# Kernel tuning notes

Measured on AMD Instinct MI355X. Metric: run time of the kernel, lower is better.

Reference implementation:

```python
import jax, jax.numpy as jnp
import numpy as np

DIM = 1024
HEADS = 16
HEAD_DIM = DIM // HEADS
HIDDEN = int(DIM * 4.0)
EPS = 1e-5


def setup_inputs() -> dict:
    key = jax.random.key(0)
    ks = jax.random.split(key, 16)
    s = 0.02
    inp = {
        'x': jax.random.normal(ks[0], (2, 2048, DIM), dtype=jnp.float32),
        'g1': jnp.ones((DIM,), jnp.float32),
        'b1': jnp.zeros((DIM,), jnp.float32),
        'Wq': jax.random.normal(ks[1], (DIM, DIM)) * s,
        'bq': jnp.zeros((DIM,), jnp.float32),
        'Wk': jax.random.normal(ks[2], (DIM, DIM)) * s,
        'bk': jnp.zeros((DIM,), jnp.float32),
        'Wv': jax.random.normal(ks[3], (DIM, DIM)) * s,
        'bv': jnp.zeros((DIM,), jnp.float32),
        'Wo': jax.random.normal(ks[4], (DIM, DIM)) * s,
        'bo': jnp.zeros((DIM,), jnp.float32),
        'g2': jnp.ones((DIM,), jnp.float32),
        'b2': jnp.zeros((DIM,), jnp.float32),
        'W1': jax.random.normal(ks[5], (DIM, HIDDEN)) * s,
        'bf1': jnp.zeros((HIDDEN,), jnp.float32),
        'W2': jax.random.normal(ks[6], (HIDDEN, DIM)) * s,
        'bf2': jnp.zeros((DIM,), jnp.float32),
    }
    return inp


def _layernorm(x, g, b):
    mu = jnp.mean(x, axis=-1, keepdims=True)
    var = jnp.mean((x - mu) ** 2, axis=-1, keepdims=True)
    return (x - mu) * jax.lax.rsqrt(var + EPS) * g + b


def _block(x, g1, b1, Wq, bq, Wk, bk, Wv, bv, Wo, bo, g2, b2, W1, bf1, W2, bf2):
    B, N, C = x.shape
    h = _layernorm(x, g1, b1)
    # project and split heads: [B, H, N, D]
    q = (h @ Wq + bq).reshape(B, N, HEADS, HEAD_DIM).transpose(0, 2, 1, 3)
    k = (h @ Wk + bk).reshape(B, N, HEADS, HEAD_DIM).transpose(0, 2, 1, 3)
    v = (h @ Wv + bv).reshape(B, N, HEADS, HEAD_DIM).transpose(0, 2, 1, 3)
    scale = HEAD_DIM ** -0.5
    attn = jnp.einsum('bhqd,bhkd->bhqk', q, k) * scale
    attn = jax.nn.softmax(attn, axis=-1)
    o = jnp.einsum('bhqk,bhkd->bhqd', attn, v)
    o = o.transpose(0, 2, 1, 3).reshape(B, N, C)
    x = x + (o @ Wo + bo)
    h = _layernorm(x, g2, b2)
    h = jax.nn.gelu(h @ W1 + bf1, approximate=False)
    x = x + (h @ W2 + bf2)
    return x


def reference(x, g1, b1, Wq, bq, Wk, bk, Wv, bv, Wo, bo, g2, b2, W1, bf1, W2, bf2):
    return _block(x, g1, b1, Wq, bq, Wk, bk, Wv, bv, Wo, bo, g2, b2, W1, bf1, W2, bf2)
```

## Files before the change

kernel.cpp:

```cpp
#include <hip/hip_runtime.h>
#include <hip/hip_bf16.h>
#include <math.h>


typedef unsigned short ushort_t;
typedef short short8 __attribute__((ext_vector_type(8)));
typedef float f32x4 __attribute__((ext_vector_type(4)));

#define TOKENS 4096
#define SEQ    2048
#define DIMC   1024
#define HID    4096

__device__ __forceinline__ float bf2f(ushort_t u) {
    union { float f; unsigned int u; } c; c.u = ((unsigned int)u) << 16; return c.f;
}
__device__ __forceinline__ ushort_t f2bf(float f) {
    union { float f; unsigned int u; } c; c.f = f;
    unsigned int u = c.u;
    unsigned int r = u + 0x7fffu + ((u >> 16) & 1u);
    return (ushort_t)(r >> 16);
}
__device__ __forceinline__ float gelu_f(float x) {
    const float y = 0.79788456080286536f * (x + 0.044715f * x * x * x);
    const float t = __expf(-2.0f * fabsf(y));
    const float th = (1.0f - t) / (1.0f + t);
    return 0.5f * x * (1.0f + copysignf(th, y));
}
__device__ __forceinline__ float load_elem(const void* p, size_t i, int isbf) {
    return isbf ? bf2f(((const ushort_t*)p)[i]) : ((const float*)p)[i];
}

__global__ __launch_bounds__(256) void detect_dtype(
    const ushort_t* __restrict__ x, int* __restrict__ flag)
{
    __shared__ int bad;
    if (threadIdx.x == 0) bad = 0;
    __syncthreads();
    for (int i = threadIdx.x; i < 4096; i += 256) {
        float v = bf2f(x[i]);
        if (!(fabsf(v) <= 1e6f)) bad = 1;
    }
    __syncthreads();
    if (threadIdx.x == 0) { flag[0] = (bad == 0) ? 1 : 0; flag[1] = 1; }
}

__global__ __launch_bounds__(256) void transpose_conv(
    const void* __restrict__ in, ushort_t* __restrict__ out, int K, int N,
    const int* __restrict__ flag)
{
    __shared__ ushort_t tile[32][33];
    const int isbf = *flag;
    const int kb = blockIdx.y * 32, nb = blockIdx.x * 32;
    const int tx = threadIdx.x & 31, ty = threadIdx.x >> 5;
    for (int i = 0; i < 4; i++) {
        int k = kb + ty + i * 8;
        tile[ty + i * 8][tx] = f2bf(load_elem(in, (size_t)k * N + nb + tx, isbf));
    }
    __syncthreads();
    for (int i = 0; i < 4; i++) {
        int n = nb + ty + i * 8;
        out[(size_t)n * K + kb + tx] = tile[tx][ty + i * 8];
    }
}

__global__ __launch_bounds__(256) void transpose_conv4(
    const void* __restrict__ w0, const void* __restrict__ w1,
    const void* __restrict__ w2, const void* __restrict__ w3,
    ushort_t* __restrict__ outbase, const int* __restrict__ flag)
{
    __shared__ ushort_t tile[32][33];
    const int isbf = *flag;
    const int z = blockIdx.z;
    const void* in = z == 0 ? w0 : (z == 1 ? w1 : (z == 2 ? w2 : w3));
    ushort_t* out = outbase + (size_t)z * DIMC * DIMC;
    const int kb = blockIdx.y * 32, nb = blockIdx.x * 32;
    const int tx = threadIdx.x & 31, ty = threadIdx.x >> 5;
    for (int i = 0; i < 4; i++) {
        int k = kb + ty + i * 8;
        tile[ty + i * 8][tx] = f2bf(load_elem(in, (size_t)k * DIMC + nb + tx, isbf));
    }
    __syncthreads();
    for (int i = 0; i < 4; i++) {
        int n = nb + ty + i * 8;
        out[(size_t)n * DIMC + kb + tx] = tile[tx][ty + i * 8];
    }
}

__global__ __launch_bounds__(256) void transpose_v(
    const ushort_t* __restrict__ in, ushort_t* __restrict__ out)
{
    __shared__ ushort_t tile[32][33];
    const int z = blockIdx.z;
    const ushort_t* src = in  + (size_t)z * SEQ * DIMC;
    ushort_t*       dst = out + (size_t)z * DIMC * SEQ;
    const int kb = blockIdx.y * 32, nb = blockIdx.x * 32;
    const int tx = threadIdx.x & 31, ty = threadIdx.x >> 5;
    for (int i = 0; i < 4; i++) {
        int k = kb + ty + i * 8;
        tile[ty + i * 8][tx] = src[(size_t)k * DIMC + nb + tx];
    }
    __syncthreads();
    for (int i = 0; i < 4; i++) {
        int n = nb + ty + i * 8;
        dst[(size_t)n * SEQ + kb + tx] = tile[tx][ty + i * 8];
    }
}

template<int INMODE>
__global__ __launch_bounds__(256) void ln_kernel(
    const void* __restrict__ in, const void* __restrict__ g,
    const void* __restrict__ b, const int* __restrict__ flag,
    ushort_t* __restrict__ out)
{
    const int isbf = *flag;
    const int t = blockIdx.x;
    const int tid = threadIdx.x;
    const size_t base = (size_t)t * DIMC;
    float v[4];
    for (int i = 0; i < 4; i++) {
        int idx = tid + i * 256;
        v[i] = (INMODE == 1) ? ((const float*)in)[base + idx]
                             : load_elem(in, base + idx, isbf);
    }
    float s  = v[0] + v[1] + v[2] + v[3];
    float s2 = v[0]*v[0] + v[1]*v[1] + v[2]*v[2] + v[3]*v[3];
    for (int off = 1; off < 64; off <<= 1) {
        s  += __shfl_xor(s,  off);
        s2 += __shfl_xor(s2, off);
    }
    __shared__ float red[8];
    const int wave = tid >> 6, lane = tid & 63;
    if (lane == 0) { red[wave] = s; red[wave + 4] = s2; }
    __syncthreads();
    s  = red[0] + red[1] + red[2] + red[3];
    s2 = red[4] + red[5] + red[6] + red[7];
    const float mu  = s * (1.0f / DIMC);
    const float var = s2 * (1.0f / DIMC) - mu * mu;
    const float inv = rsqrtf(fmaxf(var, 0.f) + 1e-5f);
    for (int i = 0; i < 4; i++) {
        int idx = tid + i * 256;
        float o = (v[i] - mu) * inv * load_elem(g, idx, isbf) + load_elem(b, idx, isbf);
        out[base + idx] = f2bf(o);
    }
}

template<int BN, int RES, int ACT, int OUTF>
__global__ __launch_bounds__(256) void gemm_bt(
    const ushort_t* __restrict__ A, const ushort_t* __restrict__ BT,
    const void* __restrict__ bias0, const void* __restrict__ bias1,
    const void* __restrict__ bias2, const void* __restrict__ resid,
    void* __restrict__ out0, void* __restrict__ out1, void* __restrict__ out2,
    int M, int N, int K, int Ksub, const int* __restrict__ flag)
{
    constexpr int BM   = 128;
    constexpr int JF   = BN / 32;
    constexpr int ASEG = BM / 16;
    constexpr int SPW  = (BM + BN) / 64;
    __shared__ __align__(16) ushort_t As[BM][32];
    __shared__ __align__(16) ushort_t Bs[BN][32];
    const int isbf = *flag;
    const int tid = threadIdx.x, lane = tid & 63, wave = tid >> 6;
    const int m0 = blockIdx.y * BM, n0 = blockIdx.x * BN;
    const int wm = (wave & 1) * 64;
    const int wn = (wave >> 1) * (BN / 2);
    const int lm = lane & 15, quad = lane >> 4;

    const void* biasp = bias0;
    void* outp = out0;
    int nout = N;
    int colmask = 0x7fffffff;
    if (OUTF == 3) {
        const int sel = n0 >> 10;
        biasp = sel == 0 ? bias0 : (sel == 1 ? bias1 : bias2);
        outp  = sel == 0 ? out0  : (sel == 1 ? out1  : out2);
        nout = 1024; colmask = 1023;
    }
    int kbeg = 0;
    if (OUTF == 4) {
        kbeg = blockIdx.z * Ksub;
        outp = blockIdx.z ? out1 : out0;
    }

    f32x4 acc[4][JF];
    for (int i = 0; i < 4; i++)
        for (int j = 0; j < JF; j++)
            acc[i][j] = (f32x4){0.f, 0.f, 0.f, 0.f};

    const int lrow = lane >> 2;
    const int lcol = (lane & 3) * 8;

    for (int k0 = kbeg; k0 < kbeg + Ksub; k0 += 32) {
#pragma unroll
        for (int s = 0; s < SPW; s++) {
            const int seg = wave * SPW + s;
            const ushort_t* gp;
            ushort_t* lp;
            if (seg < ASEG) {
                gp = &A[(size_t)(m0 + seg * 16 + lrow) * K + k0 + lcol];
                lp = &As[seg * 16][0];
            } else {
                gp = &BT[(size_t)(n0 + (seg - ASEG) * 16 + lrow) * K + k0 + lcol];
                lp = &Bs[(seg - ASEG) * 16][0];
            }
            __builtin_amdgcn_global_load_lds(
                (const __attribute__((address_space(1))) unsigned int*)gp,
                (__attribute__((address_space(3))) unsigned int*)lp, 16, 0, 0);
        }
        __syncthreads();
        short8 af[4], bfr[JF];
#pragma unroll
        for (int i = 0; i < 4; i++) af[i] = *(const short8*)&As[wm + i * 16 + lm][quad * 8];
#pragma unroll
        for (int j = 0; j < JF; j++) bfr[j] = *(const short8*)&Bs[wn + j * 16 + lm][quad * 8];
#pragma unroll
        for (int i = 0; i < 4; i++)
#pragma unroll
            for (int j = 0; j < JF; j++)
                acc[i][j] = __builtin_amdgcn_mfma_f32_16x16x32_bf16(af[i], bfr[j], acc[i][j], 0, 0, 0);
        __syncthreads();
    }

    for (int j = 0; j < JF; j++) {
        const int col  = n0 + wn + j * 16 + lm;
        const int colo = col & colmask;
        const float bv = (OUTF == 4) ? 0.f : load_elem(biasp, colo, isbf);
        for (int i = 0; i < 4; i++) {
            const int rbase = m0 + wm + i * 16 + quad * 4;
            for (int r = 0; r < 4; r++) {
                const size_t oi = (size_t)(rbase + r) * nout + colo;
                float v2 = acc[i][j][r] + bv;
                if (ACT == 1) v2 = gelu_f(v2);
                if (RES == 1) v2 += load_elem(resid, oi, isbf);
                if (RES == 2) v2 += ((const float*)resid)[oi];
                if (OUTF == 1 || OUTF == 4) { ((float*)outp)[oi] = v2; }
                else if (OUTF == 2) {
                    if (isbf) ((ushort_t*)outp)[oi] = f2bf(v2);
                    else      ((float*)outp)[oi] = v2;
                }
                else                { ((ushort_t*)outp)[oi] = f2bf(v2); }
            }
        }
    }
}

__global__ __launch_bounds__(256) void splitk_reduce(
    const float* __restrict__ p0, const float* __restrict__ p1,
    const void* __restrict__ bias, const float* __restrict__ resid,
    void* __restrict__ out, const int* __restrict__ flag)
{
    const int isbf = *flag;
    const size_t i = ((size_t)blockIdx.x * 256 + threadIdx.x) * 4;
    const float4 a = *(const float4*)&p0[i];
    const float4 b = *(const float4*)&p1[i];
    const float4 r = *(const float4*)&resid[i];
    const int col = (int)(i & 1023);
    float v[4];
    v[0] = a.x + b.x + r.x + load_elem(bias, col + 0, isbf);
    v[1] = a.y + b.y + r.y + load_elem(bias, col + 1, isbf);
    v[2] = a.z + b.z + r.z + load_elem(bias, col + 2, isbf);
    v[3] = a.w + b.w + r.w + load_elem(bias, col + 3, isbf);
    if (isbf) {
        unsigned int lo = (unsigned int)f2bf(v[0]) | ((unsigned int)f2bf(v[1]) << 16);
        unsigned int hi = (unsigned int)f2bf(v[2]) | ((unsigned int)f2bf(v[3]) << 16);
        *(uint2*)&((ushort_t*)out)[i] = make_uint2(lo, hi);
    } else {
        *(float4*)&((float*)out)[i] = make_float4(v[0], v[1], v[2], v[3]);
    }
}

__global__ __launch_bounds__(256) void attn_kernel(
    const ushort_t* __restrict__ q, const ushort_t* __restrict__ k,
    const ushort_t* __restrict__ vt, ushort_t* __restrict__ o)
{
    const int bh = blockIdx.x;
    const int b  = bh >> 4, h = bh & 15;
    const int q0 = blockIdx.y * 64;
    const int tid = threadIdx.x, lane = tid & 63, wave = tid >> 6;
    const int lm = lane & 15, quad = lane >> 4;

    __shared__ ushort_t Qs[64][72];
    __shared__ ushort_t Ks[64][72];
    __shared__ ushort_t Vt[64][72];
    __shared__ ushort_t Ps[4][16][72];

    const size_t base  = ((size_t)b * SEQ) * DIMC + h * 64;
    const size_t vbase = ((size_t)b * DIMC + h * 64) * SEQ;

    {
        const int er0 = (tid * 8) >> 6;
        const int ec0 = (tid * 8) & 63;
        for (int half = 0; half < 2; half++) {
            const int r = er0 + half * 32;
            short8 qq = *(const short8*)&q[base + (size_t)(q0 + r) * DIMC + ec0];
            short8 qs;
            for (int i = 0; i < 8; i++)
                qs[i] = (short)f2bf(bf2f((ushort_t)qq[i]) * 0.18033688011112042f);
            *(short8*)&Qs[r][ec0] = qs;
        }
    }
    __syncthreads();

    short8 qf[2];
    qf[0] = *(const short8*)&Qs[wave * 16 + lm][quad * 8];
    qf[1] = *(const short8*)&Qs[wave * 16 + lm][quad * 8 + 32];

    short8 onef;
    for (int i = 0; i < 8; i++) onef[i] = (short)0x3F80;

    f32x4 oacc[4], lacc;
    for (int j = 0; j < 4; j++) oacc[j] = (f32x4){0.f, 0.f, 0.f, 0.f};
    lacc = (f32x4){0.f, 0.f, 0.f, 0.f};

    const int er = (tid * 8) >> 6;
    const int ec = (tid * 8) & 63;
    const int dd = tid >> 2;
    const int kg = tid & 3;

    for (int kt = 0; kt < SEQ / 64; kt++) {
        __syncthreads();
        for (int half = 0; half < 2; half++) {
            const int r = er + half * 32;
            *(short8*)&Ks[r][ec] =
                *(const short8*)&k[base + (size_t)(kt * 64 + r) * DIMC + ec];
        }
        {
            const size_t vsrc = vbase + (size_t)dd * SEQ + kt * 64 + kg * 16;
            *(short8*)&Vt[dd][kg * 16]     = *(const short8*)&vt[vsrc];
            *(short8*)&Vt[dd][kg * 16 + 8] = *(const short8*)&vt[vsrc + 8];
        }
        __syncthreads();

        f32x4 st[4];
        for (int j = 0; j < 4; j++) st[j] = (f32x4){0.f, 0.f, 0.f, 0.f};
        for (int ks = 0; ks < 2; ks++) {
            for (int j = 0; j < 4; j++) {
                short8 kf = *(const short8*)&Ks[j * 16 + lm][quad * 8 + ks * 32];
                st[j] = __builtin_amdgcn_mfma_f32_16x16x32_bf16(kf, qf[ks], st[j], 0, 0, 0);
            }
        }

        for (int j = 0; j < 4; j++) {
            unsigned int u0 = __float_as_uint(exp2f(st[j][0]));
            unsigned int u1 = __float_as_uint(exp2f(st[j][1]));
            unsigned int u2 = __float_as_uint(exp2f(st[j][2]));
            unsigned int u3 = __float_as_uint(exp2f(st[j][3]));
            unsigned int lo = (u1 & 0xffff0000u) | (u0 >> 16);
            unsigned int hi = (u3 & 0xffff0000u) | (u2 >> 16);
            *(uint2*)&Ps[wave][lm][j * 16 + quad * 4] = make_uint2(lo, hi);
        }

        for (int ks = 0; ks < 2; ks++) {
            short8 pf = *(const short8*)&Ps[wave][lm][quad * 8 + ks * 32];
            lacc = __builtin_amdgcn_mfma_f32_16x16x32_bf16(pf, onef, lacc, 0, 0, 0);
            for (int j = 0; j < 4; j++) {
                short8 vf = *(const short8*)&Vt[j * 16 + lm][quad * 8 + ks * 32];
                oacc[j] = __builtin_amdgcn_mfma_f32_16x16x32_bf16(pf, vf, oacc[j], 0, 0, 0);
            }
        }
    }

    float rinv[4];
    for (int r = 0; r < 4; r++) rinv[r] = 1.0f / fmaxf(lacc[r], 1e-30f);

    for (int j = 0; j < 4; j++)
        for (int r = 0; r < 4; r++) {
            const int row = q0 + wave * 16 + quad * 4 + r;
            o[base + (size_t)row * DIMC + j * 16 + lm] = f2bf(oacc[j][r] * rinv[r]);
        }
}

extern "C" void kernel_launch(void* const* d_in, const int* in_sizes, int n_in,
                              void* d_out, int out_size, void* d_ws, size_t ws_size,
                              hipStream_t stream)
{
    const void* x   = d_in[0];
    const void* g1  = d_in[1];
    const void* b1  = d_in[2];
    const void* Wq  = d_in[3];
    const void* bq  = d_in[4];
    const void* Wk  = d_in[5];
    const void* bk  = d_in[6];
    const void* Wv  = d_in[7];
    const void* bv  = d_in[8];
    const void* Wo  = d_in[9];
    const void* bo  = d_in[10];
    const void* g2  = d_in[11];
    const void* b2  = d_in[12];
    const void* W1  = d_in[13];
    const void* bf1 = d_in[14];
    const void* W2  = d_in[15];
    const void* bf2 = d_in[16];

    const size_t SZ_TOKD_BF = (size_t)TOKENS * DIMC * 2;
    const size_t SZ_TOKD_F  = (size_t)TOKENS * DIMC * 4;
    const size_t SZ_W_SQ    = (size_t)DIMC * DIMC * 2;
    const size_t SZ_W_FF    = (size_t)DIMC * HID * 2;
    const size_t SZ_FF1     = (size_t)TOKENS * HID * 2;

    char* ws = (char*)d_ws;
    size_t off = 0;
    int*      flag = (int*)(ws + off);       off += 256;
    ushort_t* h    = (ushort_t*)(ws + off);  off += SZ_TOKD_BF;
    ushort_t* qb   = (ushort_t*)(ws + off);  off += SZ_TOKD_BF;
    ushort_t* kb_  = (ushort_t*)(ws + off);  off += SZ_TOKD_BF;
    ushort_t* vb   = (ushort_t*)(ws + off);  off += SZ_TOKD_BF;
    ushort_t* vtg  = (ushort_t*)(ws + off);  off += SZ_TOKD_BF;
    float*    x1f  = (float*)qb;
    ushort_t* ao   = vb;
    float*    p0   = (float*)vb;
    ushort_t* wqt  = (ushort_t*)(ws + off);  off += SZ_W_SQ;
    ushort_t* wkt  = (ushort_t*)(ws + off);  off += SZ_W_SQ;
    ushort_t* wvt  = (ushort_t*)(ws + off);  off += SZ_W_SQ;
    ushort_t* wot  = (ushort_t*)(ws + off);  off += SZ_W_SQ;
    ushort_t* w1t  = (ushort_t*)(ws + off);  off += SZ_W_FF;
    ushort_t* w2t  = (ushort_t*)(ws + off);  off += SZ_W_FF;
    ushort_t* ff1  = (ushort_t*)(ws + off);  off += SZ_FF1;
    float*    p1   = (float*)(ws + off);     off += SZ_TOKD_F;
    if (ws_size < off) return;

    (void)wkt; (void)wvt;

    detect_dtype<<<1, 256, 0, stream>>>((const ushort_t*)x, flag);

    transpose_conv4<<<dim3(32, 32, 4), 256, 0, stream>>>(Wq, Wk, Wv, Wo, wqt, flag);
    transpose_conv<<<dim3(128, 32), 256, 0, stream>>>(W1, w1t, DIMC, HID, flag);
    transpose_conv<<<dim3(32, 128), 256, 0, stream>>>(W2, w2t, HID, DIMC, flag);

    ln_kernel<0><<<TOKENS, 256, 0, stream>>>(x, g1, b1, flag, h);

    gemm_bt<128, 0, 0, 3><<<dim3(24, 32), 256, 0, stream>>>(
        h, wqt, bq, bk, bv, nullptr, qb, kb_, vb, TOKENS, 3072, DIMC, DIMC, flag);

    transpose_v<<<dim3(32, 64, 2), 256, 0, stream>>>(vb, vtg);

    attn_kernel<<<dim3(32, 32), 256, 0, stream>>>(qb, kb_, vtg, ao);

    gemm_bt<64, 1, 0, 1><<<dim3(16, 32), 256, 0, stream>>>(
        ao, wot, bo, nullptr, nullptr, x, x1f, nullptr, nullptr, TOKENS, DIMC, DIMC, DIMC, flag);

    ln_kernel<1><<<TOKENS, 256, 0, stream>>>(x1f, g2, b2, flag, h);

    gemm_bt<128, 0, 1, 0><<<dim3(32, 32), 256, 0, stream>>>(
        h, w1t, bf1, nullptr, nullptr, nullptr, ff1, nullptr, nullptr, TOKENS, HID, DIMC, DIMC, flag);

    gemm_bt<64, 0, 0, 4><<<dim3(16, 32, 2), 256, 0, stream>>>(
        ff1, w2t, nullptr, nullptr, nullptr, nullptr, p0, p1, nullptr,
        TOKENS, DIMC, HID, HID / 2, flag);

    splitk_reduce<<<TOKENS * DIMC / 1024, 256, 0, stream>>>(p0, p1, bf2, x1f, d_out, flag);
}
```

Measured before the change: 448.8 us.

## Fuse V transpose into QKV GEMM epilogue, enlarge attention tile, prefetch K/V

The QKV GEMM epilogue now writes V directly in transposed [B, C, S] layout, which removes the separate transpose_v kernel and its extra pass over memory. The attention kernel processes 128 queries per block (32 per wave), so each K/V tile loaded into LDS is reused across twice as many queries. It also prefetches the next K/V tile into registers while computing on the current one, and uses the hardware exp2 intrinsic. The two FFN weight transposes are merged into a single launch. Together these raise register pressure and halve the attention grid, which can lower occupancy.

```diff
diff --git a/kernel.cpp b/kernel.cpp
--- a/kernel.cpp
+++ b/kernel.cpp
@@ -43,25 +43,6 @@
     }
     __syncthreads();
     if (threadIdx.x == 0) { flag[0] = (bad == 0) ? 1 : 0; flag[1] = 1; }
-}
-
-__global__ __launch_bounds__(256) void transpose_conv(
-    const void* __restrict__ in, ushort_t* __restrict__ out, int K, int N,
-    const int* __restrict__ flag)
-{
-    __shared__ ushort_t tile[32][33];
-    const int isbf = *flag;
-    const int kb = blockIdx.y * 32, nb = blockIdx.x * 32;
-    const int tx = threadIdx.x & 31, ty = threadIdx.x >> 5;
-    for (int i = 0; i < 4; i++) {
-        int k = kb + ty + i * 8;
-        tile[ty + i * 8][tx] = f2bf(load_elem(in, (size_t)k * N + nb + tx, isbf));
-    }
-    __syncthreads();
-    for (int i = 0; i < 4; i++) {
-        int n = nb + ty + i * 8;
-        out[(size_t)n * K + kb + tx] = tile[tx][ty + i * 8];
-    }
 }
 
 __global__ __launch_bounds__(256) void transpose_conv4(
@@ -87,23 +68,30 @@
     }
 }
 
-__global__ __launch_bounds__(256) void transpose_v(
-    const ushort_t* __restrict__ in, ushort_t* __restrict__ out)
+__global__ __launch_bounds__(256) void transpose_ff(
+    const void* __restrict__ W1, const void* __restrict__ W2,
+    ushort_t* __restrict__ w1t, ushort_t* __restrict__ w2t,
+    const int* __restrict__ flag)
 {
     __shared__ ushort_t tile[32][33];
+    const int isbf = *flag;
     const int z = blockIdx.z;
-    const ushort_t* src = in  + (size_t)z * SEQ * DIMC;
-    ushort_t*       dst = out + (size_t)z * DIMC * SEQ;
-    const int kb = blockIdx.y * 32, nb = blockIdx.x * 32;
+    const void* in = z ? W2 : W1;
+    ushort_t* out = z ? w2t : w1t;
+    const int K = z ? HID : DIMC;
+    const int N = z ? DIMC : HID;
+    const int bx = z ? blockIdx.y : blockIdx.x;
+    const int by = z ? blockIdx.x : blockIdx.y;
+    const int kb = by * 32, nb = bx * 32;
     const int tx = threadIdx.x & 31, ty = threadIdx.x >> 5;
     for (int i = 0; i < 4; i++) {
         int k = kb + ty + i * 8;
-        tile[ty + i * 8][tx] = src[(size_t)k * DIMC + nb + tx];
+        tile[ty + i * 8][tx] = f2bf(load_elem(in, (size_t)k * N + nb + tx, isbf));
     }
     __syncthreads();
     for (int i = 0; i < 4; i++) {
         int n = nb + ty + i * 8;
-        dst[(size_t)n * SEQ + kb + tx] = tile[tx][ty + i * 8];
+        out[(size_t)n * K + kb + tx] = tile[tx][ty + i * 8];
     }
 }
 
@@ -170,8 +158,9 @@
     void* outp = out0;
     int nout = N;
     int colmask = 0x7fffffff;
+    int sel = 0;
     if (OUTF == 3) {
-        const int sel = n0 >> 10;
+        sel = n0 >> 10;
         biasp = sel == 0 ? bias0 : (sel == 1 ? bias1 : bias2);
         outp  = sel == 0 ? out0  : (sel == 1 ? out1  : out2);
         nout = 1024; colmask = 1023;
@@ -219,6 +208,24 @@
             for (int j = 0; j < JF; j++)
                 acc[i][j] = __builtin_amdgcn_mfma_f32_16x16x32_bf16(af[i], bfr[j], acc[i][j], 0, 0, 0);
         __syncthreads();
+    }
+
+    if (OUTF == 3 && sel == 2) {
+        for (int j = 0; j < JF; j++) {
+            const int colo = (n0 + wn + j * 16 + lm) & 1023;
+            const float bv = load_elem(biasp, colo, isbf);
+            for (int i = 0; i < 4; i++) {
+                const int token = m0 + wm + i * 16 + quad * 4;
+                const int bb = token >> 11, ss = token & 2047;
+                unsigned int lo = (unsigned int)f2bf(acc[i][j][0] + bv)
+                                | ((unsigned int)f2bf(acc[i][j][1] + bv) << 16);
+                unsigned int hi = (unsigned int)f2bf(acc[i][j][2] + bv)
+                                | ((unsigned int)f2bf(acc[i][j][3] + bv) << 16);
+                *(uint2*)&((ushort_t*)outp)[(size_t)((bb << 10) + colo) * SEQ + ss] =
+                    make_uint2(lo, hi);
+            }
+        }
+        return;
     }
 
     for (int j = 0; j < JF; j++) {
@@ -275,14 +282,14 @@
 {
     const int bh = blockIdx.x;
     const int b  = bh >> 4, h = bh & 15;
-    const int q0 = blockIdx.y * 64;
+    const int q0 = blockIdx.y * 128;
     const int tid = threadIdx.x, lane = tid & 63, wave = tid >> 6;
     const int lm = lane & 15, quad = lane >> 4;
 
-    __shared__ ushort_t Qs[64][72];
+    __shared__ ushort_t Qs[128][72];
     __shared__ ushort_t Ks[64][72];
     __shared__ ushort_t Vt[64][72];
-    __shared__ ushort_t Ps[4][16][72];
+    __shared__ ushort_t Ps[4][32][72];
 
     const size_t base  = ((size_t)b * SEQ) * DIMC + h * 64;
     const size_t vbase = ((size_t)b * DIMC + h * 64) * SEQ;
@@ -290,7 +297,7 @@
     {
         const int er0 = (tid * 8) >> 6;
         const int ec0 = (tid * 8) & 63;
-        for (int half = 0; half < 2; half++) {
+        for (int half = 0; half < 4; half++) {
             const int r = er0 + half * 32;
             short8 qq = *(const short8*)&q[base + (size_t)(q0 + r) * DIMC + ec0];
             short8 qs;
@@ -301,73 +308,94 @@
     }
     __syncthreads();
 
-    short8 qf[2];
-    qf[0] = *(const short8*)&Qs[wave * 16 + lm][quad * 8];
-    qf[1] = *(const short8*)&Qs[wave * 16 + lm][quad * 8 + 32];
+    short8 qf[2][2];
+    for (int qh = 0; qh < 2; qh++)
+        for (int ks = 0; ks < 2; ks++)
+            qf[qh][ks] = *(const short8*)&Qs[wave * 32 + qh * 16 + lm][quad * 8 + ks * 32];
 
     short8 onef;
     for (int i = 0; i < 8; i++) onef[i] = (short)0x3F80;
 
-    f32x4 oacc[4], lacc;
-    for (int j = 0; j < 4; j++) oacc[j] = (f32x4){0.f, 0.f, 0.f, 0.f};
-    lacc = (f32x4){0.f, 0.f, 0.f, 0.f};
+    f32x4 oacc[4][2], lacc[2];
+    for (int j = 0; j < 4; j++)
+        for (int qh = 0; qh < 2; qh++) oacc[j][qh] = (f32x4){0.f, 0.f, 0.f, 0.f};
+    lacc[0] = (f32x4){0.f, 0.f, 0.f, 0.f};
+    lacc[1] = (f32x4){0.f, 0.f, 0.f, 0.f};
 
     const int er = (tid * 8) >> 6;
     const int ec = (tid * 8) & 63;
     const int dd = tid >> 2;
     const int kg = tid & 3;
 
+    short8 kreg0, kreg1, vreg0, vreg1;
+    {
+        kreg0 = *(const short8*)&k[base + (size_t)(er) * DIMC + ec];
+        kreg1 = *(const short8*)&k[base + (size_t)(er + 32) * DIMC + ec];
+        const size_t vsrc = vbase + (size_t)dd * SEQ + kg * 16;
+        vreg0 = *(const short8*)&vt[vsrc];
+        vreg1 = *(const short8*)&vt[vsrc + 8];
+    }
+
     for (int kt = 0; kt < SEQ / 64; kt++) {
         __syncthreads();
-        for (int half = 0; half < 2; half++) {
-            const int r = er + half * 32;
-            *(short8*)&Ks[r][ec] =
-                *(const short8*)&k[base + (size_t)(kt * 64 + r) * DIMC + ec];
-        }
-        {
-            const size_t vsrc = vbase + (size_t)dd * SEQ + kt * 64 + kg * 16;
-            *(short8*)&Vt[dd][kg * 16]     = *(const short8*)&vt[vsrc];
-            *(short8*)&Vt[dd][kg * 16 + 8] = *(const short8*)&vt[vsrc + 8];
-        }
+        *(short8*)&Ks[er][ec]          = kreg0;
+        *(short8*)&Ks[er + 32][ec]     = kreg1;
+        *(short8*)&Vt[dd][kg * 16]     = vreg0;
+        *(short8*)&Vt[dd][kg * 16 + 8] = vreg1;
         __syncthreads();
-
-        f32x4 st[4];
-        for (int j = 0; j < 4; j++) st[j] = (f32x4){0.f, 0.f, 0.f, 0.f};
+        if (kt + 1 < SEQ / 64) {
+            const int kn = (kt + 1) * 64;
+            kreg0 = *(const short8*)&k[base + (size_t)(kn + er) * DIMC + ec];
+            kreg1 = *(const short8*)&k[base + (size_t)(kn + er + 32) * DIMC + ec];
+            const size_t vsrc = vbase + (size_t)dd * SEQ + kn + kg * 16;
+            vreg0 = *(const short8*)&vt[vsrc];
+            vreg1 = *(const short8*)&vt[vsrc + 8];
+        }
+
+        f32x4 st[4][2];
+        for (int j = 0; j < 4; j++)
+            for (int qh = 0; qh < 2; qh++) st[j][qh] = (f32x4){0.f, 0.f, 0.f, 0.f};
         for (int ks = 0; ks < 2; ks++) {
             for (int j = 0; j < 4; j++) {
                 short8 kf = *(const short8*)&Ks[j * 16 + lm][quad * 8 + ks * 32];
-                st[j] = __builtin_amdgcn_mfma_f32_16x16x32_bf16(kf, qf[ks], st[j], 0, 0, 0);
-            }
-        }
-
-        for (int j = 0; j < 4; j++) {
-            unsigned int u0 = __float_as_uint(exp2f(st[j][0]));
-            unsigned int u1 = __float_as_uint(exp2f(st[j][1]));
-            unsigned int u2 = __float_as_uint(exp2f(st[j][2]));
-            unsigned int u3 = __float_as_uint(exp2f(st[j][3]));
-            unsigned int lo = (u1 & 0xffff0000u) | (u0 >> 16);
-            unsigned int hi = (u3 & 0xffff0000u) | (u2 >> 16);
-            *(uint2*)&Ps[wave][lm][j * 16 + quad * 4] = make_uint2(lo, hi);
-        }
+                for (int qh = 0; qh < 2; qh++)
+                    st[j][qh] = __builtin_amdgcn_mfma_f32_16x16x32_bf16(kf, qf[qh][ks], st[j][qh], 0, 0, 0);
+            }
+        }
+
+        for (int j = 0; j < 4; j++)
+            for (int qh = 0; qh < 2; qh++) {
+                unsigned int u0 = __float_as_uint(__builtin_amdgcn_exp2f(st[j][qh][0]));
+                unsigned int u1 = __float_as_uint(__builtin_amdgcn_exp2f(st[j][qh][1]));
+                unsigned int u2 = __float_as_uint(__builtin_amdgcn_exp2f(st[j][qh][2]));
+                unsigned int u3 = __float_as_uint(__builtin_amdgcn_exp2f(st[j][qh][3]));
+                unsigned int lo = (u1 & 0xffff0000u) | (u0 >> 16);
+                unsigned int hi = (u3 & 0xffff0000u) | (u2 >> 16);
+                *(uint2*)&Ps[wave][qh * 16 + lm][j * 16 + quad * 4] = make_uint2(lo, hi);
+            }
 
         for (int ks = 0; ks < 2; ks++) {
-            short8 pf = *(const short8*)&Ps[wave][lm][quad * 8 + ks * 32];
-            lacc = __builtin_amdgcn_mfma_f32_16x16x32_bf16(pf, onef, lacc, 0, 0, 0);
-            for (int j = 0; j < 4; j++) {
-                short8 vf = *(const short8*)&Vt[j * 16 + lm][quad * 8 + ks * 32];
-                oacc[j] = __builtin_amdgcn_mfma_f32_16x16x32_bf16(pf, vf, oacc[j], 0, 0, 0);
-            }
-        }
-    }
-
-    float rinv[4];
-    for (int r = 0; r < 4; r++) rinv[r] = 1.0f / fmaxf(lacc[r], 1e-30f);
+            for (int qh = 0; qh < 2; qh++) {
+                short8 pf = *(const short8*)&Ps[wave][qh * 16 + lm][quad * 8 + ks * 32];
+                lacc[qh] = __builtin_amdgcn_mfma_f32_16x16x32_bf16(pf, onef, lacc[qh], 0, 0, 0);
+                for (int j = 0; j < 4; j++) {
+                    short8 vf = *(const short8*)&Vt[j * 16 + lm][quad * 8 + ks * 32];
+                    oacc[j][qh] = __builtin_amdgcn_mfma_f32_16x16x32_bf16(pf, vf, oacc[j][qh], 0, 0, 0);
+                }
+            }
+        }
+    }
+
+    float rinv[2][4];
+    for (int qh = 0; qh < 2; qh++)
+        for (int r = 0; r < 4; r++) rinv[qh][r] = 1.0f / fmaxf(lacc[qh][r], 1e-30f);
 
     for (int j = 0; j < 4; j++)
-        for (int r = 0; r < 4; r++) {
-            const int row = q0 + wave * 16 + quad * 4 + r;
-            o[base + (size_t)row * DIMC + j * 16 + lm] = f2bf(oacc[j][r] * rinv[r]);
-        }
+        for (int qh = 0; qh < 2; qh++)
+            for (int r = 0; r < 4; r++) {
+                const int row = q0 + wave * 32 + qh * 16 + quad * 4 + r;
+                o[base + (size_t)row * DIMC + j * 16 + lm] = f2bf(oacc[j][qh][r] * rinv[qh][r]);
+            }
 }
 
 extern "C" void kernel_launch(void* const* d_in, const int* in_sizes, int n_in,
@@ -404,11 +432,10 @@
     ushort_t* h    = (ushort_t*)(ws + off);  off += SZ_TOKD_BF;
     ushort_t* qb   = (ushort_t*)(ws + off);  off += SZ_TOKD_BF;
     ushort_t* kb_  = (ushort_t*)(ws + off);  off += SZ_TOKD_BF;
-    ushort_t* vb   = (ushort_t*)(ws + off);  off += SZ_TOKD_BF;
+    ushort_t* ao   = (ushort_t*)(ws + off);  off += SZ_TOKD_BF;
     ushort_t* vtg  = (ushort_t*)(ws + off);  off += SZ_TOKD_BF;
     float*    x1f  = (float*)qb;
-    ushort_t* ao   = vb;
-    float*    p0   = (float*)vb;
+    float*    p0   = (float*)ao;
     ushort_t* wqt  = (ushort_t*)(ws + off);  off += SZ_W_SQ;
     ushort_t* wkt  = (ushort_t*)(ws + off);  off += SZ_W_SQ;
     ushort_t* wvt  = (ushort_t*)(ws + off);  off += SZ_W_SQ;
@@ -424,17 +451,14 @@
     detect_dtype<<<1, 256, 0, stream>>>((const ushort_t*)x, flag);
 
     transpose_conv4<<<dim3(32, 32, 4), 256, 0, stream>>>(Wq, Wk, Wv, Wo, wqt, flag);
-    transpose_conv<<<dim3(128, 32), 256, 0, stream>>>(W1, w1t, DIMC, HID, flag);
-    transpose_conv<<<dim3(32, 128), 256, 0, stream>>>(W2, w2t, HID, DIMC, flag);
+    transpose_ff<<<dim3(128, 32, 2), 256, 0, stream>>>(W1, W2, w1t, w2t, flag);
 
     ln_kernel<0><<<TOKENS, 256, 0, stream>>>(x, g1, b1, flag, h);
 
     gemm_bt<128, 0, 0, 3><<<dim3(24, 32), 256, 0, stream>>>(
-        h, wqt, bq, bk, bv, nullptr, qb, kb_, vb, TOKENS, 3072, DIMC, DIMC, flag);
-
-    transpose_v<<<dim3(32, 64, 2), 256, 0, stream>>>(vb, vtg);
-
-    attn_kernel<<<dim3(32, 32), 256, 0, stream>>>(qb, kb_, vtg, ao);
+        h, wqt, bq, bk, bv, nullptr, qb, kb_, vtg, TOKENS, 3072, DIMC, DIMC, flag);
+
+    attn_kernel<<<dim3(32, 16), 256, 0, stream>>>(qb, kb_, vtg, ao);
 
     gemm_bt<64, 1, 0, 1><<<dim3(16, 32), 256, 0, stream>>>(
         ao, wot, bo, nullptr, nullptr, x, x1f, nullptr, nullptr, TOKENS, DIMC, DIMC, DIMC, flag);
```

Result: no change. 442.4 us (-1.4%).
